# Performance work log

Measured on AMD Instinct MI355X. Metric: run time of the kernel, lower is better.

The kernel has to match this reference:

```python
import jax, jax.numpy as jnp
import numpy as np

B, S, D, H = 4, 2048, 1024, 16
DK = D // H
NEG = -1.0e9

def setup_inputs() -> dict:
    key = jax.random.key(0)
    ks = jax.random.split(key, 9)
    scale = 1.0 / np.sqrt(D)
    x = jax.random.normal(ks[0], (B, S, D), dtype=jnp.float32)
    # causal mask: positions with mask==0 are filled with -1e9
    mask = jnp.tril(jnp.ones((S, S), dtype=jnp.int32))[None, None]  # [1,1,S,S]
    Wq = jax.random.normal(ks[1], (D, D), dtype=jnp.float32) * scale
    bq = jax.random.normal(ks[2], (D,), dtype=jnp.float32) * 0.01
    Wk = jax.random.normal(ks[3], (D, D), dtype=jnp.float32) * scale
    bk = jax.random.normal(ks[4], (D,), dtype=jnp.float32) * 0.01
    Wv = jax.random.normal(ks[5], (D, D), dtype=jnp.float32) * scale
    bv = jax.random.normal(ks[6], (D,), dtype=jnp.float32) * 0.01
    Wo = jax.random.normal(ks[7], (D, D), dtype=jnp.float32) * scale
    bo = jax.random.normal(ks[8], (D,), dtype=jnp.float32) * 0.01
    return {"x": x, "mask": mask, "Wq": Wq, "bq": bq, "Wk": Wk, "bk": bk,
            "Wv": Wv, "bv": bv, "Wo": Wo, "bo": bo}

def reference(x, mask, Wq, bq, Wk, bk, Wv, bv, Wo, bo):
    Bb, Ss, Dd = x.shape
    q = (x @ Wq.T + bq).reshape(Bb, Ss, H, DK).transpose(0, 2, 1, 3)  # [B,H,S,DK]
    k = (x @ Wk.T + bk).reshape(Bb, Ss, H, DK).transpose(0, 2, 1, 3)
    v = (x @ Wv.T + bv).reshape(Bb, Ss, H, DK).transpose(0, 2, 1, 3)
    scaled = jnp.einsum('bhqd,bhkd->bhqk', q, k) / jnp.sqrt(jnp.float32(DK))
    scaled = jnp.where(mask == 0, jnp.float32(NEG), scaled)
    attn = jax.nn.softmax(scaled, axis=-1)  # dropout prob = 0 -> identity
    vals = jnp.einsum('bhqk,bhkd->bhqd', attn, v)  # [B,H,S,DK]
    vals = vals.transpose(0, 2, 1, 3).reshape(Bb, Ss, H * DK)
    out = vals @ Wo.T + bo
    return out
```

## Files before the change

kernel.cpp:

```cpp
#include <hip/hip_runtime.h>
#include <hip/hip_bf16.h>
#include <cstdint>

#define B_ 4
#define S_ 2048
#define D_ 1024
#define H_ 16
#define DK_ 64

typedef _Float16 h8 __attribute__((ext_vector_type(8)));
typedef _Float16 h4 __attribute__((ext_vector_type(4)));
typedef _Float16 h2 __attribute__((ext_vector_type(2)));
typedef float f32x4 __attribute__((ext_vector_type(4)));
typedef unsigned int u32x4 __attribute__((ext_vector_type(4)));

__device__ __forceinline__ void gload16(const void* src, void* lds) {
  __builtin_amdgcn_global_load_lds((const __attribute__((address_space(1))) void*)src,
                                   (__attribute__((address_space(3))) void*)lds, 16, 0, 0);
}

__global__ __launch_bounds__(256) void conv_all(
    const float* __restrict__ x,
    const float* __restrict__ Wq, const float* __restrict__ Wk,
    const float* __restrict__ Wv, const float* __restrict__ Wo,
    const float* __restrict__ bq, const float* __restrict__ bk,
    const float* __restrict__ bv,
    _Float16* __restrict__ xb, _Float16* __restrict__ wqkv,
    _Float16* __restrict__ wo, float* __restrict__ bqkv) {
  const int bid = blockIdx.x, tid = threadIdx.x;
  if (bid < 4096) {
    int base = (bid * 256 + tid) * 8;
    h8 o;
#pragma unroll
    for (int j = 0; j < 8; ++j) o[j] = (_Float16)x[base + j];
    *(h8*)(xb + base) = o;
  } else {
    int i = (bid - 4096) * 256 + tid;
    int seg = i >> 17, r = i & 131071;
    const float* src = seg == 0 ? Wq : seg == 1 ? Wk : seg == 2 ? Wv : Wo;
    int base = r * 8;
    h8 o;
#pragma unroll
    for (int j = 0; j < 8; ++j) o[j] = (_Float16)src[base + j];
    if (seg < 3)
      *(h8*)(wqkv + (size_t)seg * 1048576 + base) = o;
    else
      *(h8*)(wo + base) = o;
    if (i < 768) {
      int bsel = i >> 8, k = (i & 255) * 4;
      const float* bs = bsel == 0 ? bq : bsel == 1 ? bk : bv;
      float4 v = *(const float4*)(bs + k);
      *(float4*)(bqkv + bsel * 1024 + k) = v;
    }
  }
}

template <int MODE>
__global__ __launch_bounds__(256) void gemm_nt(const _Float16* __restrict__ A,
                                               const _Float16* __restrict__ Bw,
                                               const float* __restrict__ bias,
                                               void* __restrict__ Cout,
                                               _Float16* __restrict__ Vt) {
  constexpr int K = D_;
  __shared__ unsigned short lds[2 * 128 * 64];
  char* ldsA = (char*)lds;
  char* ldsB = (char*)(lds + 128 * 64);

  const int tid = threadIdx.x;
  const int w = tid >> 6, lane = tid & 63, g = lane >> 4, c = lane & 15;
  const int wr = w >> 1, wc = w & 1;
  const int bn = blockIdx.x;
  const int bm = blockIdx.y;

  f32x4 acc[4][4] = {};

  const int srow = tid >> 3;
  const int scolsw = ((tid & 7) * 16) ^ ((srow & 7) << 4);
  const char* Ab = (const char*)(A + (size_t)bm * 128 * K);
  const char* Bb = (const char*)(Bw + (size_t)bn * 128 * K);
  const char* Asrc[4];
  const char* Bsrc[4];
#pragma unroll
  for (int j = 0; j < 4; ++j) {
    int row = j * 32 + srow;
    Asrc[j] = Ab + (size_t)row * (K * 2) + scolsw;
    Bsrc[j] = Bb + (size_t)row * (K * 2) + scolsw;
  }
  char* dstA = ldsA + w * 1024;
  char* dstB = ldsB + w * 1024;

  for (int k0 = 0; k0 < K; k0 += 64) {
    __syncthreads();
#pragma unroll
    for (int j = 0; j < 4; ++j) {
      gload16(Asrc[j] + k0 * 2, dstA + j * 4096);
      gload16(Bsrc[j] + k0 * 2, dstB + j * 4096);
    }
    __syncthreads();
#pragma unroll
    for (int kk = 0; kk < 2; ++kk) {
      h8 a[4], b[4];
#pragma unroll
      for (int mi = 0; mi < 4; ++mi) {
        int row = wr * 64 + mi * 16 + c;
        int off = row * 128 + kk * 64 + g * 16;
        a[mi] = *(const h8*)(ldsA + (off ^ ((row & 7) << 4)));
      }
#pragma unroll
      for (int ni = 0; ni < 4; ++ni) {
        int row = wc * 64 + ni * 16 + c;
        int off = row * 128 + kk * 64 + g * 16;
        b[ni] = *(const h8*)(ldsB + (off ^ ((row & 7) << 4)));
      }
      __builtin_amdgcn_s_setprio(1);
#pragma unroll
      for (int mi = 0; mi < 4; ++mi)
#pragma unroll
        for (int ni = 0; ni < 4; ++ni)
          acc[mi][ni] = __builtin_amdgcn_mfma_f32_16x16x32_f16(a[mi], b[ni], acc[mi][ni], 0, 0, 0);
      __builtin_amdgcn_s_setprio(0);
    }
  }

  if (MODE == 0 && bn >= 16) {
#pragma unroll
    for (int mi = 0; mi < 4; ++mi)
#pragma unroll
      for (int ni = 0; ni < 4; ++ni) {
        int m0 = bm * 128 + wr * 64 + mi * 16 + g * 4;
        int n = bn * 128 + wc * 64 + ni * 16 + c;
        float bb = bias[n];
        h4 v4;
#pragma unroll
        for (int r = 0; r < 4; ++r) v4[r] = (_Float16)(acc[mi][ni][r] + bb);
        int bI = m0 >> 11, sI = m0 & 2047;
        int dk = n & 63, hh = (n >> 6) & 15;
        *(h4*)(Vt + (((size_t)(bI * 16 + hh) * 64 + dk) * 2048 + sI)) = v4;
      }
  } else {
#pragma unroll
    for (int mi = 0; mi < 4; ++mi)
#pragma unroll
      for (int ni = 0; ni < 4; ++ni)
#pragma unroll
        for (int r = 0; r < 4; ++r) {
          int m = bm * 128 + wr * 64 + mi * 16 + g * 4 + r;
          int n = bn * 128 + wc * 64 + ni * 16 + c;
          float v = acc[mi][ni][r] + bias[n];
          if (MODE == 0) {
            int which = n >> 10, nn = n & 1023;
            int bI = m >> 11, sI = m & 2047, hI = nn >> 6, dkI = nn & 63;
            ((_Float16*)Cout)[(size_t)which * 8388608 +
                              (((size_t)bI * H_ + hI) * S_ + sI) * DK_ + dkI] = (_Float16)v;
          } else {
            ((float*)Cout)[(size_t)m * D_ + n] = v;
          }
        }
  }
}

__global__ __launch_bounds__(256) void attn_fwd(const _Float16* __restrict__ Q,
                                                const _Float16* __restrict__ K,
                                                const _Float16* __restrict__ Vt,
                                                _Float16* __restrict__ vals) {
  __shared__ unsigned short ldsK[2 * 64 * 64];
  __shared__ unsigned short ldsV[2 * 64 * 64];
  __shared__ unsigned short ldsP[4 * 16 * 64];
  char* pK = (char*)ldsK;
  char* pV = (char*)ldsV;
  char* pP = (char*)ldsP;

  const int tid = threadIdx.x;
  const int w = tid >> 6, lane = tid & 63, g = lane >> 4, c = lane & 15;
  const int bid = blockIdx.x;
  const int pi = bid >> 6;
  const int bh = bid & 63;
  const int bI = bh >> 4, hI = bh & 15;
  const int q0 = pi, q1 = 31 - pi;

  const char* Qb = (const char*)(Q + (size_t)bh * S_ * DK_);
  const char* Kb = (const char*)(K + (size_t)bh * S_ * DK_);
  const char* Vtb = (const char*)(Vt + (size_t)bh * DK_ * S_);

  const int srow = tid >> 3;
  const int scol = (tid & 7) * 16;
  int offK[2], offV[2];
#pragma unroll
  for (int j = 0; j < 2; ++j) {
    int row = j * 32 + srow;
    int colsw = scol ^ ((row & 7) << 4);
    offK[j] = row * 128 + colsw;
    offV[j] = row * 4096 + colsw;
  }
  char* dstK = pK + w * 1024;
  char* dstV = pV + w * 1024;

  auto stage = [&](int buf, int kv0) {
#pragma unroll
    for (int j = 0; j < 2; ++j) {
      gload16(Kb + (size_t)kv0 * 128 + offK[j], dstK + buf * 8192 + j * 4096);
      gload16(Vtb + (size_t)kv0 * 2 + offV[j], dstV + buf * 8192 + j * 4096);
    }
  };

  const _Float16 qsc = (_Float16)(0.125f * 1.44269504f);
  const int sw = (c & 7) << 4;

  for (int phase = 0; phase < 2; ++phase) {
    const int qsub = (phase == 0) ? q0 : q1;
    const int qw0 = qsub * 64 + w * 16;

    h8 qf[2];
#pragma unroll
    for (int kk = 0; kk < 2; ++kk) {
      h8 v = *(const h8*)(Qb + (size_t)(qw0 + c) * 128 + kk * 64 + g * 16);
#pragma unroll
      for (int j = 0; j < 8; ++j) v[j] *= qsc;
      qf[kk] = v;
    }

    f32x4 o[4] = {};
    float m_ = -1e30f, l_ = 0.f;

    const int nt = qsub + 1;
    stage(0, 0);
    __syncthreads();

    for (int t = 0; t < nt; ++t) {
      const int cur = t & 1;
      if (t + 1 < nt) stage(cur ^ 1, (t + 1) * 64);
      const char* bK = pK + cur * 8192;
      const char* bV = pV + cur * 8192;

      f32x4 s[4] = {};
#pragma unroll
      for (int kk = 0; kk < 2; ++kk) {
        h8 kfx[4];
#pragma unroll
        for (int ni = 0; ni < 4; ++ni) {
          int row = ni * 16 + c;
          kfx[ni] = *(const h8*)(bK + ((row * 128 + kk * 64 + g * 16) ^ sw));
        }
        __builtin_amdgcn_s_setprio(1);
#pragma unroll
        for (int ni = 0; ni < 4; ++ni)
          s[ni] = __builtin_amdgcn_mfma_f32_16x16x32_f16(kfx[ni], qf[kk], s[ni], 0, 0, 0);
        __builtin_amdgcn_s_setprio(0);
      }

      if (t == nt - 1) {
#pragma unroll
        for (int ni = 0; ni < 4; ++ni)
#pragma unroll
          for (int r = 0; r < 4; ++r) {
            int kv = ni * 16 + g * 4 + r;
            if (kv > w * 16 + c) s[ni][r] = -1e30f;
          }
      }

      float m4[4];
#pragma unroll
      for (int ni = 0; ni < 4; ++ni)
        m4[ni] = fmaxf(fmaxf(s[ni][0], s[ni][1]), fmaxf(s[ni][2], s[ni][3]));
      float pmax = fmaxf(fmaxf(m4[0], m4[1]), fmaxf(m4[2], m4[3]));
      if (!__all(pmax <= m_ + 8.f)) {
        float rm = fmaxf(pmax, __shfl_xor(pmax, 16));
        rm = fmaxf(rm, __shfl_xor(rm, 32));
        float mn = fmaxf(m_, rm);
        float al = __builtin_amdgcn_exp2f(m_ - mn);
        m_ = mn;
        l_ *= al;
#pragma unroll
        for (int r = 0; r < 4; ++r) {
          float alr = __shfl(al, g * 4 + r);
#pragma unroll
          for (int nd = 0; nd < 4; ++nd) o[nd][r] *= alr;
        }
      }
      const float mn = m_;
      float rs = 0.f;

#pragma unroll
      for (int ni = 0; ni < 2; ++ni) {
        float e0 = __builtin_amdgcn_exp2f(s[ni][0] - mn);
        float e1 = __builtin_amdgcn_exp2f(s[ni][1] - mn);
        float e2 = __builtin_amdgcn_exp2f(s[ni][2] - mn);
        float e3 = __builtin_amdgcn_exp2f(s[ni][3] - mn);
        rs += (e0 + e1) + (e2 + e3);
        h2 lo = __builtin_bit_cast(h2, __builtin_amdgcn_cvt_pkrtz(e0, e1));
        h2 hi = __builtin_bit_cast(h2, __builtin_amdgcn_cvt_pkrtz(e2, e3));
        h4 pk4 = {lo[0], lo[1], hi[0], hi[1]};
        int off = w * 2048 + c * 128 + ni * 32 + g * 8;
        *(h4*)(pP + (off ^ sw)) = pk4;
      }
      {
        h8 pf = *(const h8*)(pP + ((w * 2048 + c * 128 + g * 16) ^ sw));
        h8 vf[4];
#pragma unroll
        for (int nd = 0; nd < 4; ++nd) {
          int row = nd * 16 + c;
          vf[nd] = *(const h8*)(bV + ((row * 128 + g * 16) ^ sw));
        }
        __builtin_amdgcn_s_setprio(1);
#pragma unroll
        for (int nd = 0; nd < 4; ++nd)
          o[nd] = __builtin_amdgcn_mfma_f32_16x16x32_f16(pf, vf[nd], o[nd], 0, 0, 0);
        __builtin_amdgcn_s_setprio(0);
      }
#pragma unroll
      for (int ni = 2; ni < 4; ++ni) {
        float e0 = __builtin_amdgcn_exp2f(s[ni][0] - mn);
        float e1 = __builtin_amdgcn_exp2f(s[ni][1] - mn);
        float e2 = __builtin_amdgcn_exp2f(s[ni][2] - mn);
        float e3 = __builtin_amdgcn_exp2f(s[ni][3] - mn);
        rs += (e0 + e1) + (e2 + e3);
        h2 lo = __builtin_bit_cast(h2, __builtin_amdgcn_cvt_pkrtz(e0, e1));
        h2 hi = __builtin_bit_cast(h2, __builtin_amdgcn_cvt_pkrtz(e2, e3));
        h4 pk4 = {lo[0], lo[1], hi[0], hi[1]};
        int off = w * 2048 + c * 128 + ni * 32 + g * 8;
        *(h4*)(pP + (off ^ sw)) = pk4;
      }
      {
        h8 pf = *(const h8*)(pP + ((w * 2048 + c * 128 + 64 + g * 16) ^ sw));
        h8 vf[4];
#pragma unroll
        for (int nd = 0; nd < 4; ++nd) {
          int row = nd * 16 + c;
          vf[nd] = *(const h8*)(bV + ((row * 128 + 64 + g * 16) ^ sw));
        }
        __builtin_amdgcn_s_setprio(1);
#pragma unroll
        for (int nd = 0; nd < 4; ++nd)
          o[nd] = __builtin_amdgcn_mfma_f32_16x16x32_f16(pf, vf[nd], o[nd], 0, 0, 0);
        __builtin_amdgcn_s_setprio(0);
      }
      l_ += rs;

      __syncthreads();
    }

    float lt = l_ + __shfl_xor(l_, 16);
    lt += __shfl_xor(lt, 32);
    float linv = 1.0f / lt;
#pragma unroll
    for (int r = 0; r < 4; ++r) {
      float inv = __shfl(linv, g * 4 + r);
      int qrow = qsub * 64 + w * 16 + g * 4 + r;
#pragma unroll
      for (int nd = 0; nd < 4; ++nd) {
        int col = hI * 64 + nd * 16 + c;
        vals[((size_t)bI * S_ + qrow) * D_ + col] = (_Float16)(o[nd][r] * inv);
      }
    }
  }
}

extern "C" void kernel_launch(void* const* d_in, const int* in_sizes, int n_in,
                              void* d_out, int out_size, void* d_ws, size_t ws_size,
                              hipStream_t stream) {
  const float* x  = (const float*)d_in[0];
  const float* Wq = (const float*)d_in[2];
  const float* bq = (const float*)d_in[3];
  const float* Wk = (const float*)d_in[4];
  const float* bk = (const float*)d_in[5];
  const float* Wv = (const float*)d_in[6];
  const float* bv = (const float*)d_in[7];
  const float* Wo = (const float*)d_in[8];
  const float* bo = (const float*)d_in[9];
  float* out = (float*)d_out;

  char* ws = (char*)d_ws;
  size_t off = 0;
  auto alloc = [&](size_t bytes) {
    char* p = ws + off;
    off += (bytes + 255) & ~(size_t)255;
    return p;
  };
  _Float16* xb   = (_Float16*)alloc((size_t)B_ * S_ * D_ * 2);
  _Float16* wqkv = (_Float16*)alloc((size_t)3 * D_ * D_ * 2);
  _Float16* wob  = (_Float16*)alloc((size_t)D_ * D_ * 2);
  float*    bqkv = (float*)alloc((size_t)3 * D_ * 4);
  _Float16* qkvw = (_Float16*)alloc((size_t)2 * B_ * H_ * S_ * DK_ * 2);
  _Float16* Vtw  = (_Float16*)alloc((size_t)B_ * H_ * S_ * DK_ * 2);
  _Float16* valw = (_Float16*)alloc((size_t)B_ * S_ * D_ * 2);

  conv_all<<<6144, 256, 0, stream>>>(x, Wq, Wk, Wv, Wo, bq, bk, bv, xb, wqkv, wob, bqkv);

  gemm_nt<0><<<dim3(24, 64), 256, 0, stream>>>(xb, wqkv, bqkv, qkvw, Vtw);

  attn_fwd<<<1024, 256, 0, stream>>>(qkvw, qkvw + (size_t)8388608, Vtw, valw);

  gemm_nt<1><<<dim3(8, 64), 256, 0, stream>>>(valw, wob, bo, out, nullptr);
}
```

Measured before the change: 191.9 us.

## Rewrite attention with 32x32x16 MFMA, 2-wave blocks, and register-shuffled P

The attention kernel moves from 16x16x32 MFMAs with 4 waves of 16 query rows to 32x32x16 MFMAs with 2 waves of 32 query rows each, so blocks drop to 128 threads. The P matrix no longer round-trips through LDS; it is rearranged into the A-operand layout in registers using cross-half lane shuffles. On the diagonal tile, wave 0 skips the fully masked second key half. The aim is fewer LDS operations and better MFMA efficiency per tile, at the cost of more accumulator registers and fewer waves per block.

```diff
diff --git a/kernel.cpp b/kernel.cpp
--- a/kernel.cpp
+++ b/kernel.cpp
@@ -10,8 +10,8 @@
 
 typedef _Float16 h8 __attribute__((ext_vector_type(8)));
 typedef _Float16 h4 __attribute__((ext_vector_type(4)));
-typedef _Float16 h2 __attribute__((ext_vector_type(2)));
 typedef float f32x4 __attribute__((ext_vector_type(4)));
+typedef float f32x16 __attribute__((ext_vector_type(16)));
 typedef unsigned int u32x4 __attribute__((ext_vector_type(4)));
 
 __device__ __forceinline__ void gload16(const void* src, void* lds) {
@@ -159,24 +159,20 @@
   }
 }
 
-__global__ __launch_bounds__(256) void attn_fwd(const _Float16* __restrict__ Q,
+__global__ __launch_bounds__(128) void attn_fwd(const _Float16* __restrict__ Q,
                                                 const _Float16* __restrict__ K,
                                                 const _Float16* __restrict__ Vt,
                                                 _Float16* __restrict__ vals) {
-  __shared__ unsigned short ldsK[2 * 64 * 64];
-  __shared__ unsigned short ldsV[2 * 64 * 64];
-  __shared__ unsigned short ldsP[4 * 16 * 64];
-  char* pK = (char*)ldsK;
-  char* pV = (char*)ldsV;
-  char* pP = (char*)ldsP;
+  __shared__ char lds[2 * 16384];
 
   const int tid = threadIdx.x;
-  const int w = tid >> 6, lane = tid & 63, g = lane >> 4, c = lane & 15;
+  const int w = tid >> 6;
+  const int lane = tid & 63;
+  const int l31 = lane & 31, hi = lane >> 5;
   const int bid = blockIdx.x;
   const int pi = bid >> 6;
   const int bh = bid & 63;
   const int bI = bh >> 4, hI = bh & 15;
-  const int q0 = pi, q1 = 31 - pi;
 
   const char* Qb = (const char*)(Q + (size_t)bh * S_ * DK_);
   const char* Kb = (const char*)(K + (size_t)bh * S_ * DK_);
@@ -184,173 +180,182 @@
 
   const int srow = tid >> 3;
   const int scol = (tid & 7) * 16;
-  int offK[2], offV[2];
-#pragma unroll
-  for (int j = 0; j < 2; ++j) {
-    int row = j * 32 + srow;
+  int offK[4], offV[4];
+#pragma unroll
+  for (int j = 0; j < 4; ++j) {
+    int row = j * 16 + srow;
     int colsw = scol ^ ((row & 7) << 4);
     offK[j] = row * 128 + colsw;
     offV[j] = row * 4096 + colsw;
   }
-  char* dstK = pK + w * 1024;
-  char* dstV = pV + w * 1024;
-
-  auto stage = [&](int buf, int kv0) {
-#pragma unroll
-    for (int j = 0; j < 2; ++j) {
-      gload16(Kb + (size_t)kv0 * 128 + offK[j], dstK + buf * 8192 + j * 4096);
-      gload16(Vtb + (size_t)kv0 * 2 + offV[j], dstV + buf * 8192 + j * 4096);
-    }
-  };
+
+  int rdo[4];
+#pragma unroll
+  for (int ks = 0; ks < 4; ++ks)
+    rdo[ks] = l31 * 128 + ((ks * 32 + hi * 16) ^ ((l31 & 7) << 4));
 
   const _Float16 qsc = (_Float16)(0.125f * 1.44269504f);
-  const int sw = (c & 7) << 4;
 
   for (int phase = 0; phase < 2; ++phase) {
-    const int qsub = (phase == 0) ? q0 : q1;
-    const int qw0 = qsub * 64 + w * 16;
-
-    h8 qf[2];
-#pragma unroll
-    for (int kk = 0; kk < 2; ++kk) {
-      h8 v = *(const h8*)(Qb + (size_t)(qw0 + c) * 128 + kk * 64 + g * 16);
+    const int p64 = (phase == 0) ? pi : 31 - pi;
+    const int qs32 = p64 * 2 + w;
+    const int nt = p64 + 1;
+
+    h8 qf[4];
+#pragma unroll
+    for (int ks = 0; ks < 4; ++ks) {
+      h8 v = *(const h8*)(Qb + (size_t)(qs32 * 32 + l31) * 128 + ks * 32 + hi * 16);
 #pragma unroll
       for (int j = 0; j < 8; ++j) v[j] *= qsc;
-      qf[kk] = v;
-    }
-
-    f32x4 o[4] = {};
+      qf[ks] = v;
+    }
+
+    f32x16 o[2] = {};
     float m_ = -1e30f, l_ = 0.f;
 
-    const int nt = qsub + 1;
-    stage(0, 0);
+#pragma unroll
+    for (int j = 0; j < 4; ++j) {
+      gload16(Kb + offK[j], lds + j * 2048 + w * 1024);
+      gload16(Vtb + offV[j], lds + 8192 + j * 2048 + w * 1024);
+    }
     __syncthreads();
 
     for (int t = 0; t < nt; ++t) {
       const int cur = t & 1;
-      if (t + 1 < nt) stage(cur ^ 1, (t + 1) * 64);
-      const char* bK = pK + cur * 8192;
-      const char* bV = pV + cur * 8192;
-
-      f32x4 s[4] = {};
-#pragma unroll
-      for (int kk = 0; kk < 2; ++kk) {
-        h8 kfx[4];
-#pragma unroll
-        for (int ni = 0; ni < 4; ++ni) {
-          int row = ni * 16 + c;
-          kfx[ni] = *(const h8*)(bK + ((row * 128 + kk * 64 + g * 16) ^ sw));
-        }
+      const char* ldsb = lds + cur * 16384;
+      if (t + 1 < nt) {
+        const size_t kvo = (size_t)(t + 1) * 64;
+        char* nb = lds + (cur ^ 1) * 16384;
+#pragma unroll
+        for (int j = 0; j < 4; ++j) {
+          gload16(Kb + kvo * 128 + offK[j], nb + j * 2048 + w * 1024);
+          gload16(Vtb + kvo * 2 + offV[j], nb + 8192 + j * 2048 + w * 1024);
+        }
+      }
+
+      const bool diag = (t == nt - 1);
+      const bool skip1 = diag && (w == 0);
+
+      f32x16 s0 = {}, s1 = {};
+#pragma unroll
+      for (int ks = 0; ks < 4; ++ks) {
+        h8 k0 = *(const h8*)(ldsb + rdo[ks]);
+        h8 k1 = *(const h8*)(ldsb + 4096 + rdo[ks]);
         __builtin_amdgcn_s_setprio(1);
-#pragma unroll
-        for (int ni = 0; ni < 4; ++ni)
-          s[ni] = __builtin_amdgcn_mfma_f32_16x16x32_f16(kfx[ni], qf[kk], s[ni], 0, 0, 0);
+        s0 = __builtin_amdgcn_mfma_f32_32x32x16_f16(k0, qf[ks], s0, 0, 0, 0);
+        if (!skip1) s1 = __builtin_amdgcn_mfma_f32_32x32x16_f16(k1, qf[ks], s1, 0, 0, 0);
         __builtin_amdgcn_s_setprio(0);
       }
 
-      if (t == nt - 1) {
-#pragma unroll
-        for (int ni = 0; ni < 4; ++ni)
-#pragma unroll
-          for (int r = 0; r < 4; ++r) {
-            int kv = ni * 16 + g * 4 + r;
-            if (kv > w * 16 + c) s[ni][r] = -1e30f;
+      if (diag) {
+        if (w == 0) {
+#pragma unroll
+          for (int r = 0; r < 16; ++r) {
+            int rowidx = (r & 3) + 8 * (r >> 2) + 4 * hi;
+            if (rowidx > l31) s0[r] = -1e30f;
           }
-      }
-
-      float m4[4];
-#pragma unroll
-      for (int ni = 0; ni < 4; ++ni)
-        m4[ni] = fmaxf(fmaxf(s[ni][0], s[ni][1]), fmaxf(s[ni][2], s[ni][3]));
-      float pmax = fmaxf(fmaxf(m4[0], m4[1]), fmaxf(m4[2], m4[3]));
+        } else {
+#pragma unroll
+          for (int r = 0; r < 16; ++r) {
+            int rowidx = (r & 3) + 8 * (r >> 2) + 4 * hi;
+            if (rowidx > l31) s1[r] = -1e30f;
+          }
+        }
+      }
+
+      float t8[8];
+#pragma unroll
+      for (int j = 0; j < 8; ++j) t8[j] = fmaxf(s0[2 * j], s0[2 * j + 1]);
+      if (!skip1)
+#pragma unroll
+        for (int j = 0; j < 8; ++j) t8[j] = fmaxf(t8[j], fmaxf(s1[2 * j], s1[2 * j + 1]));
+      float t4a = fmaxf(t8[0], t8[1]), t4b = fmaxf(t8[2], t8[3]);
+      float t4c = fmaxf(t8[4], t8[5]), t4d = fmaxf(t8[6], t8[7]);
+      float pmax = fmaxf(fmaxf(t4a, t4b), fmaxf(t4c, t4d));
+
       if (!__all(pmax <= m_ + 8.f)) {
-        float rm = fmaxf(pmax, __shfl_xor(pmax, 16));
-        rm = fmaxf(rm, __shfl_xor(rm, 32));
+        float rm = fmaxf(pmax, __shfl_xor(pmax, 32));
         float mn = fmaxf(m_, rm);
         float al = __builtin_amdgcn_exp2f(m_ - mn);
         m_ = mn;
         l_ *= al;
 #pragma unroll
-        for (int r = 0; r < 4; ++r) {
-          float alr = __shfl(al, g * 4 + r);
-#pragma unroll
-          for (int nd = 0; nd < 4; ++nd) o[nd][r] *= alr;
-        }
-      }
-      const float mn = m_;
-      float rs = 0.f;
-
-#pragma unroll
-      for (int ni = 0; ni < 2; ++ni) {
-        float e0 = __builtin_amdgcn_exp2f(s[ni][0] - mn);
-        float e1 = __builtin_amdgcn_exp2f(s[ni][1] - mn);
-        float e2 = __builtin_amdgcn_exp2f(s[ni][2] - mn);
-        float e3 = __builtin_amdgcn_exp2f(s[ni][3] - mn);
-        rs += (e0 + e1) + (e2 + e3);
-        h2 lo = __builtin_bit_cast(h2, __builtin_amdgcn_cvt_pkrtz(e0, e1));
-        h2 hi = __builtin_bit_cast(h2, __builtin_amdgcn_cvt_pkrtz(e2, e3));
-        h4 pk4 = {lo[0], lo[1], hi[0], hi[1]};
-        int off = w * 2048 + c * 128 + ni * 32 + g * 8;
-        *(h4*)(pP + (off ^ sw)) = pk4;
-      }
-      {
-        h8 pf = *(const h8*)(pP + ((w * 2048 + c * 128 + g * 16) ^ sw));
-        h8 vf[4];
-#pragma unroll
-        for (int nd = 0; nd < 4; ++nd) {
-          int row = nd * 16 + c;
-          vf[nd] = *(const h8*)(bV + ((row * 128 + g * 16) ^ sw));
-        }
-        __builtin_amdgcn_s_setprio(1);
-#pragma unroll
-        for (int nd = 0; nd < 4; ++nd)
-          o[nd] = __builtin_amdgcn_mfma_f32_16x16x32_f16(pf, vf[nd], o[nd], 0, 0, 0);
-        __builtin_amdgcn_s_setprio(0);
-      }
-#pragma unroll
-      for (int ni = 2; ni < 4; ++ni) {
-        float e0 = __builtin_amdgcn_exp2f(s[ni][0] - mn);
-        float e1 = __builtin_amdgcn_exp2f(s[ni][1] - mn);
-        float e2 = __builtin_amdgcn_exp2f(s[ni][2] - mn);
-        float e3 = __builtin_amdgcn_exp2f(s[ni][3] - mn);
-        rs += (e0 + e1) + (e2 + e3);
-        h2 lo = __builtin_bit_cast(h2, __builtin_amdgcn_cvt_pkrtz(e0, e1));
-        h2 hi = __builtin_bit_cast(h2, __builtin_amdgcn_cvt_pkrtz(e2, e3));
-        h4 pk4 = {lo[0], lo[1], hi[0], hi[1]};
-        int off = w * 2048 + c * 128 + ni * 32 + g * 8;
-        *(h4*)(pP + (off ^ sw)) = pk4;
-      }
-      {
-        h8 pf = *(const h8*)(pP + ((w * 2048 + c * 128 + 64 + g * 16) ^ sw));
-        h8 vf[4];
-#pragma unroll
-        for (int nd = 0; nd < 4; ++nd) {
-          int row = nd * 16 + c;
-          vf[nd] = *(const h8*)(bV + ((row * 128 + 64 + g * 16) ^ sw));
-        }
-        __builtin_amdgcn_s_setprio(1);
-#pragma unroll
-        for (int nd = 0; nd < 4; ++nd)
-          o[nd] = __builtin_amdgcn_mfma_f32_16x16x32_f16(pf, vf[nd], o[nd], 0, 0, 0);
-        __builtin_amdgcn_s_setprio(0);
-      }
-      l_ += rs;
+        for (int r = 0; r < 16; ++r) {
+          float av = __shfl(al, (r & 3) + 8 * (r >> 2) + 4 * hi);
+          o[0][r] *= av;
+          o[1][r] *= av;
+        }
+      }
+
+      unsigned int u0[8], u1[8];
+      float rsa = 0.f, rsb = 0.f;
+#pragma unroll
+      for (int j = 0; j < 8; ++j) {
+        float e0 = __builtin_amdgcn_exp2f(s0[2 * j] - m_);
+        float e1 = __builtin_amdgcn_exp2f(s0[2 * j + 1] - m_);
+        rsa += e0 + e1;
+        u0[j] = __builtin_bit_cast(unsigned int, __builtin_amdgcn_cvt_pkrtz(e0, e1));
+      }
+      if (!skip1) {
+#pragma unroll
+        for (int j = 0; j < 8; ++j) {
+          float e0 = __builtin_amdgcn_exp2f(s1[2 * j] - m_);
+          float e1 = __builtin_amdgcn_exp2f(s1[2 * j + 1] - m_);
+          rsb += e0 + e1;
+          u1[j] = __builtin_bit_cast(unsigned int, __builtin_amdgcn_cvt_pkrtz(e0, e1));
+        }
+      }
+      l_ += rsa + rsb;
+
+      h8 pa0[2], pa1[2];
+#pragma unroll
+      for (int b = 0; b < 2; ++b) {
+        unsigned int ua = u0[4 * b], ub = u0[4 * b + 1];
+        unsigned int uc = u0[4 * b + 2], ud = u0[4 * b + 3];
+        unsigned int va = hi ? ua : uc, vb = hi ? ub : ud;
+        unsigned int xa = __shfl_xor(va, 32), xb = __shfl_xor(vb, 32);
+        u32x4 q = {hi ? xa : ua, hi ? xb : ub, hi ? uc : xa, hi ? ud : xb};
+        pa0[b] = __builtin_bit_cast(h8, q);
+      }
+      if (!skip1) {
+#pragma unroll
+        for (int b = 0; b < 2; ++b) {
+          unsigned int ua = u1[4 * b], ub = u1[4 * b + 1];
+          unsigned int uc = u1[4 * b + 2], ud = u1[4 * b + 3];
+          unsigned int va = hi ? ua : uc, vb = hi ? ub : ud;
+          unsigned int xa = __shfl_xor(va, 32), xb = __shfl_xor(vb, 32);
+          u32x4 q = {hi ? xa : ua, hi ? xb : ub, hi ? uc : xa, hi ? ud : xb};
+          pa1[b] = __builtin_bit_cast(h8, q);
+        }
+      }
+
+#pragma unroll
+      for (int x = 0; x < 2; ++x) {
+#pragma unroll
+        for (int kvs = 0; kvs < 4; ++kvs) {
+          int ni = kvs >> 1, b = kvs & 1;
+          if (skip1 && ni == 1) continue;
+          h8 vf = *(const h8*)(ldsb + 8192 + x * 4096 + rdo[kvs]);
+          h8 pa = ni ? pa1[b] : pa0[b];
+          __builtin_amdgcn_s_setprio(1);
+          o[x] = __builtin_amdgcn_mfma_f32_32x32x16_f16(pa, vf, o[x], 0, 0, 0);
+          __builtin_amdgcn_s_setprio(0);
+        }
+      }
 
       __syncthreads();
     }
 
-    float lt = l_ + __shfl_xor(l_, 16);
-    lt += __shfl_xor(lt, 32);
+    float lt = l_ + __shfl_xor(l_, 32);
     float linv = 1.0f / lt;
 #pragma unroll
-    for (int r = 0; r < 4; ++r) {
-      float inv = __shfl(linv, g * 4 + r);
-      int qrow = qsub * 64 + w * 16 + g * 4 + r;
-#pragma unroll
-      for (int nd = 0; nd < 4; ++nd) {
-        int col = hI * 64 + nd * 16 + c;
-        vals[((size_t)bI * S_ + qrow) * D_ + col] = (_Float16)(o[nd][r] * inv);
-      }
+    for (int r = 0; r < 16; ++r) {
+      int qidx = (r & 3) + 8 * (r >> 2) + 4 * hi;
+      float inv = __shfl(linv, qidx);
+      int qrow = qs32 * 32 + qidx;
+      size_t rowoff = ((size_t)bI * S_ + qrow) * D_ + hI * 64 + l31;
+      vals[rowoff] = (_Float16)(o[0][r] * inv);
+      vals[rowoff + 32] = (_Float16)(o[1][r] * inv);
     }
   }
 }
@@ -388,7 +393,7 @@
 
   gemm_nt<0><<<dim3(24, 64), 256, 0, stream>>>(xb, wqkv, bqkv, qkvw, Vtw);
 
-  attn_fwd<<<1024, 256, 0, stream>>>(qkvw, qkvw + (size_t)8388608, Vtw, valw);
+  attn_fwd<<<1024, 128, 0, stream>>>(qkvw, qkvw + (size_t)8388608, Vtw, valw);
 
   gemm_nt<1><<<dim3(8, 64), 256, 0, stream>>>(valw, wob, bo, out, nullptr);
 }
```

New measurement: 209.0 us. 1.09x slower.
